# Kernel tuning notes

Measured on AMD Instinct MI355X. Metric: run time of the kernel, lower is better.

Reference implementation:

```python
import jax, jax.numpy as jnp
import numpy as np

B, S, DIM = 4, 2048, 2048
H, KVH, HD = 32, 8, 64
REPEATS = H // KVH
SCALE = HD ** -0.5


def _rope(x, cos, sin):
    # x: (B, S, Hn, HD); cos/sin: (S, HD//2)
    xr = x[..., 0::2]
    xi = x[..., 1::2]
    c = cos[:, None, :]  # (S, 1, HD//2) broadcasts over heads
    s = sin[:, None, :]
    out_r = xr * c - xi * s
    out_i = xr * s + xi * c
    return jnp.stack([out_r, out_i], axis=-1).reshape(x.shape)


def setup_inputs() -> dict:
    key = jax.random.key(0)
    ks = jax.random.split(key, 5)
    x = jax.random.normal(ks[0], (B, S, DIM), dtype=jnp.float32)
    wq = jax.random.normal(ks[1], (H * HD, DIM), dtype=jnp.float32) * 0.02
    wk = jax.random.normal(ks[2], (KVH * HD, DIM), dtype=jnp.float32) * 0.02
    wv = jax.random.normal(ks[3], (KVH * HD, DIM), dtype=jnp.float32) * 0.02
    wo = jax.random.normal(ks[4], (DIM, H * HD), dtype=jnp.float32) * 0.02
    # standard RoPE frequencies: freqs_cis = exp(i * t * theta)
    inv_freq = 1.0 / (10000.0 ** (jnp.arange(0, HD, 2, dtype=jnp.float32) / HD))
    angles = jnp.arange(S, dtype=jnp.float32)[:, None] * inv_freq[None, :]  # (S, HD//2)
    return {
        "x": x, "wq": wq, "wk": wk, "wv": wv, "wo": wo,
        "freqs_cos": jnp.cos(angles), "freqs_sin": jnp.sin(angles),
    }


def reference(x, wq, wk, wv, wo, freqs_cos, freqs_sin):
    b, s, _ = x.shape
    q = (x @ wq.T).reshape(b, s, H, HD)
    k = (x @ wk.T).reshape(b, s, KVH, HD)
    v = (x @ wv.T).reshape(b, s, KVH, HD)
    q = _rope(q, freqs_cos, freqs_sin)
    k = _rope(k, freqs_cos, freqs_sin)
    k_rep = jnp.repeat(k, REPEATS, axis=2)  # (B,S,H,HD)
    v_rep = jnp.repeat(v, REPEATS, axis=2)
    # NOTE: faithful to source - q is NOT transposed to (B,H,S,HD), so the
    # matmul contracts head_dim at each token, producing (B,S,H,H) scores
    # (mixing across heads per position), softmaxed over the last head axis.
    scores = jnp.einsum('bshd,bsed->bshe', q, k_rep) * SCALE  # (B,S,H,H)
    weights = jax.nn.softmax(scores, axis=-1)
    out = jnp.einsum('bshe,bsed->bshd', weights, v_rep)  # (B,S,H,HD)
    out = out.reshape(b, s, H * HD)
    return out @ wo.T
```

## Files before the change

kernel.cpp:

```cpp
#include <hip/hip_runtime.h>

typedef unsigned short u16;
typedef __bf16 bf16x8 __attribute__((ext_vector_type(8)));
typedef float f32x4 __attribute__((ext_vector_type(4)));

#define AS1 __attribute__((address_space(1)))
#define AS3 __attribute__((address_space(3)))

__device__ inline u16 f2bf(float f) {
    union { float f; unsigned u; } c; c.f = f;
    unsigned u = c.u;
    u += 0x7fffu + ((u >> 16) & 1u);
    return (u16)(u >> 16);
}
__device__ inline float bf2f(u16 b) {
    union { unsigned u; float f; } c; c.u = ((unsigned)b) << 16;
    return c.f;
}

__device__ inline void async_cp16(const void* g, void* l) {
    __builtin_amdgcn_global_load_lds((const AS1 void*)g, (AS3 void*)l, 16, 0, 0);
}

__global__ __launch_bounds__(256)
void f32_to_bf16_x8(const float* __restrict__ src, u16* __restrict__ dst) {
    int i = (blockIdx.x * 256 + threadIdx.x) * 8;
    float4 f0 = *(const float4*)(src + i);
    float4 f1 = *(const float4*)(src + i + 4);
    union { u16 h[8]; uint4 v; } o;
    o.h[0] = f2bf(f0.x); o.h[1] = f2bf(f0.y);
    o.h[2] = f2bf(f0.z); o.h[3] = f2bf(f0.w);
    o.h[4] = f2bf(f1.x); o.h[5] = f2bf(f1.y);
    o.h[6] = f2bf(f1.z); o.h[7] = f2bf(f1.w);
    *(uint4*)(dst + i) = o.v;
}

__global__ __launch_bounds__(256)
void conv_weights(const float* __restrict__ wq, const float* __restrict__ wk,
                  const float* __restrict__ wv, const float* __restrict__ wo,
                  u16* __restrict__ wqkv, u16* __restrict__ wo_bf) {
    int i = (blockIdx.x * 256 + threadIdx.x) * 4;
    const float* src;
    u16* dst;
    if (i < 4194304)       { src = wq + i;           dst = wqkv + i; }
    else if (i < 5242880)  { src = wk + (i-4194304); dst = wqkv + i; }
    else if (i < 6291456)  { src = wv + (i-5242880); dst = wqkv + i; }
    else                   { src = wo + (i-6291456); dst = wo_bf + (i-6291456); }
    float4 f = *(const float4*)src;
    union { u16 h[4]; uint2 v; } o;
    o.h[0] = f2bf(f.x); o.h[1] = f2bf(f.y);
    o.h[2] = f2bf(f.z); o.h[3] = f2bf(f.w);
    *(uint2*)dst = o.v;
}

template <bool BF16_OUT>
__global__ __launch_bounds__(512, 2)
void gemm_bt8(const u16* __restrict__ A, const u16* __restrict__ B,
              void* __restrict__ Cout, int N, int K) {
    __shared__ __align__(16) u16 lds[65536];
    char* ldsc = (char*)lds;

    const int tid  = threadIdx.x;
    const int w    = tid >> 6;
    const int lane = tid & 63;
    const int row0 = blockIdx.x * 256;
    const int col0 = blockIdx.y * 256;
    const int wm = w >> 2, wn = w & 3;
    const int lm = lane & 15, quad = lane >> 4;

    const int NT  = K / 64;
    const int NIT = K / 128;
    const int K64 = K * 64, K128 = K * 128;

    const int sr  = lane >> 3;
    const int stC = ((lane & 7) ^ sr) * 8;
    const u16* pA = A + (size_t)(row0 + w * 8 + sr) * K + stC;
    const u16* pB = B + (size_t)(col0 + w * 8 + sr) * K + stC;
    const int stagoff = w * 1024;

    const int cx0   = (quad ^ (lm & 7)) * 16;
    const int cx1   = cx0 ^ 64;
    const int aBase = (wm * 128 + lm) * 128;
    const int bBase = 32768 + (wn * 64 + lm) * 128;

    f32x4 acc[8][4];
#pragma unroll
    for (int i = 0; i < 8; i++)
#pragma unroll
        for (int j = 0; j < 4; j++) acc[i][j] = (f32x4){0.f, 0.f, 0.f, 0.f};

    auto stA = [&](int v, int h) {
        int kb = (v < NT ? v : NT - 1) * 64;
        const u16* g = pA + h * K128 + kb;
        char* d = ldsc + ((v & 1) << 16) + h * 16384 + stagoff;
        async_cp16(g, d);
        async_cp16(g + K64, d + 8192);
    };
    auto stB = [&](int v, int h) {
        int kb = (v < NT ? v : NT - 1) * 64;
        const u16* g = pB + h * K128 + kb;
        char* d = ldsc + ((v & 1) << 16) + 32768 + h * 16384 + stagoff;
        async_cp16(g, d);
        async_cp16(g + K64, d + 8192);
    };

    stB(0, 0); stB(0, 1); stA(0, 0); stA(0, 1);
    stB(1, 0); stB(1, 1); stA(1, 0);
    asm volatile("s_waitcnt vmcnt(6)" ::: "memory");
    __builtin_amdgcn_s_barrier();

    bf16x8 bg[4][2], afX[2][2], afY[2][2];

#define LDR(off) (*(const bf16x8*)(ldsc + (off)))

#define PHASE_TAIL(MI0, AF)                                                   \
    __builtin_amdgcn_s_barrier();                                             \
    asm volatile("s_waitcnt lgkmcnt(0)" ::: "memory");                        \
    __builtin_amdgcn_sched_barrier(0);                                        \
    __builtin_amdgcn_s_setprio(1);                                            \
    _Pragma("unroll")                                                         \
    for (int s = 0; s < 2; s++)                                               \
        _Pragma("unroll")                                                     \
        for (int j = 0; j < 2; j++)                                           \
            _Pragma("unroll")                                                 \
            for (int ni = 0; ni < 4; ni++)                                    \
                acc[(MI0) + j][ni] = __builtin_amdgcn_mfma_f32_16x16x32_bf16( \
                    AF[j][s], bg[ni][s], acc[(MI0) + j][ni], 0, 0, 0);        \
    __builtin_amdgcn_s_setprio(0);

#define HALF_ITER(u, BO)                                                      \
    {                                                                         \
                                                                      \
        _Pragma("unroll")                                                     \
        for (int ni = 0; ni < 4; ni++) {                                      \
            bg[ni][0] = LDR((BO) + bBase + ni * 2048 + cx0);                  \
            bg[ni][1] = LDR((BO) + bBase + ni * 2048 + cx1);                  \
        }                                                                     \
        _Pragma("unroll")                                                     \
        for (int j = 0; j < 2; j++) {                                         \
            afX[j][0] = LDR((BO) + aBase + j * 2048 + cx0);                   \
            afX[j][1] = LDR((BO) + aBase + j * 2048 + cx1);                   \
            afY[j][0] = LDR((BO) + aBase + (2 + j) * 2048 + cx0);             \
            afY[j][1] = LDR((BO) + aBase + (2 + j) * 2048 + cx1);             \
        }                                                                     \
        stA((u) + 1, 1);                                                      \
        asm volatile("s_waitcnt lgkmcnt(8)" ::: "memory");                    \
        PHASE_TAIL(0, afX)                                                    \
        __builtin_amdgcn_s_barrier();                                         \
                                                                      \
        _Pragma("unroll")                                                     \
        for (int j = 0; j < 2; j++) {                                         \
            afX[j][0] = LDR((BO) + aBase + (4 + j) * 2048 + cx0);             \
            afX[j][1] = LDR((BO) + aBase + (4 + j) * 2048 + cx1);             \
        }                                                                     \
        stB((u) + 2, 0);                                                      \
        PHASE_TAIL(2, afY)                                                    \
        __builtin_amdgcn_s_barrier();                                         \
                                                                      \
        _Pragma("unroll")                                                     \
        for (int j = 0; j < 2; j++) {                                         \
            afY[j][0] = LDR((BO) + aBase + (6 + j) * 2048 + cx0);             \
            afY[j][1] = LDR((BO) + aBase + (6 + j) * 2048 + cx1);             \
        }                                                                     \
        stB((u) + 2, 1);                                                      \
        PHASE_TAIL(4, afX)                                                    \
        __builtin_amdgcn_s_barrier();                                         \
                                                                      \
        stA((u) + 2, 0);                                                      \
        PHASE_TAIL(6, afY)                                                    \
        asm volatile("s_waitcnt vmcnt(6)" ::: "memory");                      \
        __builtin_amdgcn_s_barrier();                                         \
    }

    for (int it = 0; it < NIT; ++it) {
        const int t = 2 * it;
        HALF_ITER(t, 0)
        HALF_ITER(t + 1, 65536)
    }

#undef HALF_ITER
#undef PHASE_TAIL
#undef LDR

    const int rbase = row0 + wm * 128 + quad * 4;
    const int cbase = col0 + wn * 64 + lm;
    if (BF16_OUT) {
        u16* C = (u16*)Cout;
#pragma unroll
        for (int mi = 0; mi < 8; mi++)
#pragma unroll
            for (int r = 0; r < 4; r++) {
                size_t ro = (size_t)(rbase + mi * 16 + r) * N;
#pragma unroll
                for (int ni = 0; ni < 4; ni++)
                    C[ro + cbase + ni * 16] = f2bf(acc[mi][ni][r]);
            }
    } else {
        float* C = (float*)Cout;
#pragma unroll
        for (int mi = 0; mi < 8; mi++)
#pragma unroll
            for (int r = 0; r < 4; r++) {
                size_t ro = (size_t)(rbase + mi * 16 + r) * N;
#pragma unroll
                for (int ni = 0; ni < 4; ni++)
                    C[ro + cbase + ni * 16] = acc[mi][ni][r];
            }
    }
}

__global__ __launch_bounds__(256)
void attn_tok(const u16* __restrict__ qkv, u16* __restrict__ out) {
    __shared__ float kvf[1024];
    const int tok = blockIdx.x;
    const int t = threadIdx.x;
    const u16* qrow = qkv + (size_t)tok * 3072;

    {
        uint2 w = *(const uint2*)(qrow + 2048 + t * 4);
        kvf[t * 4 + 0] = bf2f((u16)(w.x & 0xffff));
        kvf[t * 4 + 1] = bf2f((u16)(w.x >> 16));
        kvf[t * 4 + 2] = bf2f((u16)(w.y & 0xffff));
        kvf[t * 4 + 3] = bf2f((u16)(w.y >> 16));
    }
    __syncthreads();

    const int h = t >> 3, j = t & 7;
    float qf[8];
    {
        uint4 w = *(const uint4*)(qrow + h * 64 + j * 8);
        unsigned ws4[4] = {w.x, w.y, w.z, w.w};
#pragma unroll
        for (int i = 0; i < 4; i++) {
            qf[2 * i]     = bf2f((u16)(ws4[i] & 0xffff));
            qf[2 * i + 1] = bf2f((u16)(ws4[i] >> 16));
        }
    }

    float s[8];
#pragma unroll
    for (int g = 0; g < 8; g++) {
        const float* kk = kvf + g * 64 + j * 8;
        float a = 0.f;
#pragma unroll
        for (int d = 0; d < 8; d++) a += qf[d] * kk[d];
        s[g] = a;
    }
#pragma unroll
    for (int g = 0; g < 8; g++) {
        s[g] += __shfl_xor(s[g], 1);
        s[g] += __shfl_xor(s[g], 2);
        s[g] += __shfl_xor(s[g], 4);
    }
    float m = -1e30f;
#pragma unroll
    for (int g = 0; g < 8; g++) { s[g] *= 0.125f; m = fmaxf(m, s[g]); }
    float p[8], l = 0.f;
#pragma unroll
    for (int g = 0; g < 8; g++) { p[g] = __expf(s[g] - m); l += p[g]; }
    float rl = 1.f / l;

    float o[8] = {0, 0, 0, 0, 0, 0, 0, 0};
#pragma unroll
    for (int g = 0; g < 8; g++) {
        float w = p[g] * rl;
        const float* vv = kvf + 512 + g * 64 + j * 8;
#pragma unroll
        for (int d = 0; d < 8; d++) o[d] += w * vv[d];
    }

    unsigned po[4];
#pragma unroll
    for (int i = 0; i < 4; i++)
        po[i] = (unsigned)f2bf(o[2 * i]) | ((unsigned)f2bf(o[2 * i + 1]) << 16);
    uint4 wo_; wo_.x = po[0]; wo_.y = po[1]; wo_.z = po[2]; wo_.w = po[3];
    *(uint4*)(out + (size_t)tok * 2048 + h * 64 + j * 8) = wo_;
}

extern "C" void kernel_launch(void* const* d_in, const int* in_sizes, int n_in,
                              void* d_out, int out_size, void* d_ws, size_t ws_size,
                              hipStream_t stream) {
    const float* x  = (const float*)d_in[0];
    const float* wq = (const float*)d_in[1];
    const float* wk = (const float*)d_in[2];
    const float* wv = (const float*)d_in[3];
    const float* wo = (const float*)d_in[4];

    u16* x_bf  = (u16*)d_ws;
    u16* wqkv  = x_bf  + 16777216;
    u16* wo_bf = wqkv  + 6291456;
    u16* qkv   = wo_bf + 4194304;
    u16* attn  = qkv   + 25165824;

    f32_to_bf16_x8<<<8192, dim3(256), 0, stream>>>(x, x_bf);
    conv_weights<<<10240, dim3(256), 0, stream>>>(wq, wk, wv, wo, wqkv, wo_bf);

    gemm_bt8<true><<<dim3(32, 12), dim3(512), 0, stream>>>(x_bf, wqkv, qkv, 3072, 2048);

    attn_tok<<<8192, dim3(256), 0, stream>>>(qkv, attn);

    gemm_bt8<false><<<dim3(32, 8), dim3(512), 0, stream>>>(attn, wo_bf, (float*)d_out,
                                                           2048, 2048);
}
```

Before: 340.0 us.

## Parametrize GEMM N-tile width and merge conversion kernels into one launch

Result: faster. 328.9 us (-3.3%).

```diff
diff --git a/kernel.cpp b/kernel.cpp
--- a/kernel.cpp
+++ b/kernel.cpp
@@ -23,54 +23,56 @@
 }
 
 __global__ __launch_bounds__(256)
-void f32_to_bf16_x8(const float* __restrict__ src, u16* __restrict__ dst) {
-    int i = (blockIdx.x * 256 + threadIdx.x) * 8;
-    float4 f0 = *(const float4*)(src + i);
-    float4 f1 = *(const float4*)(src + i + 4);
-    union { u16 h[8]; uint4 v; } o;
-    o.h[0] = f2bf(f0.x); o.h[1] = f2bf(f0.y);
-    o.h[2] = f2bf(f0.z); o.h[3] = f2bf(f0.w);
-    o.h[4] = f2bf(f1.x); o.h[5] = f2bf(f1.y);
-    o.h[6] = f2bf(f1.z); o.h[7] = f2bf(f1.w);
-    *(uint4*)(dst + i) = o.v;
-}
-
-__global__ __launch_bounds__(256)
-void conv_weights(const float* __restrict__ wq, const float* __restrict__ wk,
-                  const float* __restrict__ wv, const float* __restrict__ wo,
-                  u16* __restrict__ wqkv, u16* __restrict__ wo_bf) {
-    int i = (blockIdx.x * 256 + threadIdx.x) * 4;
-    const float* src;
-    u16* dst;
-    if (i < 4194304)       { src = wq + i;           dst = wqkv + i; }
-    else if (i < 5242880)  { src = wk + (i-4194304); dst = wqkv + i; }
-    else if (i < 6291456)  { src = wv + (i-5242880); dst = wqkv + i; }
-    else                   { src = wo + (i-6291456); dst = wo_bf + (i-6291456); }
-    float4 f = *(const float4*)src;
-    union { u16 h[4]; uint2 v; } o;
-    o.h[0] = f2bf(f.x); o.h[1] = f2bf(f.y);
-    o.h[2] = f2bf(f.z); o.h[3] = f2bf(f.w);
-    *(uint2*)dst = o.v;
-}
-
-template <bool BF16_OUT>
+void conv_all(const float* __restrict__ x,
+              const float* __restrict__ wq, const float* __restrict__ wk,
+              const float* __restrict__ wv, const float* __restrict__ wo,
+              u16* __restrict__ x_bf, u16* __restrict__ wqkv,
+              u16* __restrict__ wo_bf) {
+    int b = blockIdx.x;
+    if (b < 8192) {
+        int i = (b * 256 + threadIdx.x) * 8;
+        float4 f0 = *(const float4*)(x + i);
+        float4 f1 = *(const float4*)(x + i + 4);
+        union { u16 h[8]; uint4 v; } o;
+        o.h[0] = f2bf(f0.x); o.h[1] = f2bf(f0.y);
+        o.h[2] = f2bf(f0.z); o.h[3] = f2bf(f0.w);
+        o.h[4] = f2bf(f1.x); o.h[5] = f2bf(f1.y);
+        o.h[6] = f2bf(f1.z); o.h[7] = f2bf(f1.w);
+        *(uint4*)(x_bf + i) = o.v;
+    } else {
+        int i = ((b - 8192) * 256 + threadIdx.x) * 4;
+        const float* src;
+        u16* dst;
+        if (i < 4194304)       { src = wq + i;           dst = wqkv + i; }
+        else if (i < 5242880)  { src = wk + (i-4194304); dst = wqkv + i; }
+        else if (i < 6291456)  { src = wv + (i-5242880); dst = wqkv + i; }
+        else                   { src = wo + (i-6291456); dst = wo_bf + (i-6291456); }
+        float4 f = *(const float4*)src;
+        union { u16 h[4]; uint2 v; } o;
+        o.h[0] = f2bf(f.x); o.h[1] = f2bf(f.y);
+        o.h[2] = f2bf(f.z); o.h[3] = f2bf(f.w);
+        *(uint2*)dst = o.v;
+    }
+}
+
+template <int NI, bool BF16_OUT>
 __global__ __launch_bounds__(512, 2)
 void gemm_bt8(const u16* __restrict__ A, const u16* __restrict__ B,
               void* __restrict__ Cout, int N, int K) {
-    __shared__ __align__(16) u16 lds[65536];
-    char* ldsc = (char*)lds;
+    constexpr int SZ = 32768 + NI * 8192;
+    __shared__ __align__(16) char ldsc[2 * SZ];
 
     const int tid  = threadIdx.x;
     const int w    = tid >> 6;
     const int lane = tid & 63;
     const int row0 = blockIdx.x * 256;
-    const int col0 = blockIdx.y * 256;
+    const int col0 = blockIdx.y * (NI * 64);
     const int wm = w >> 2, wn = w & 3;
     const int lm = lane & 15, quad = lane >> 4;
 
     const int NT  = K / 64;
     const int NIT = K / 128;
-    const int K64 = K * 64, K128 = K * 128;
+    const int K64 = K * 64;
 
     const int sr  = lane >> 3;
     const int stC = ((lane & 7) ^ sr) * 8;
@@ -81,35 +83,34 @@
     const int cx0   = (quad ^ (lm & 7)) * 16;
     const int cx1   = cx0 ^ 64;
     const int aBase = (wm * 128 + lm) * 128;
-    const int bBase = 32768 + (wn * 64 + lm) * 128;
-
-    f32x4 acc[8][4];
+    const int bBase = 32768 + (wn * (NI * 16) + lm) * 128;
+
+    f32x4 acc[8][NI];
 #pragma unroll
     for (int i = 0; i < 8; i++)
 #pragma unroll
-        for (int j = 0; j < 4; j++) acc[i][j] = (f32x4){0.f, 0.f, 0.f, 0.f};
-
-    auto stA = [&](int v, int h) {
+        for (int j = 0; j < NI; j++) acc[i][j] = (f32x4){0.f, 0.f, 0.f, 0.f};
+
+    auto stage = [&](const u16* base, int v, int unit, int regionOff) {
         int kb = (v < NT ? v : NT - 1) * 64;
-        const u16* g = pA + h * K128 + kb;
-        char* d = ldsc + ((v & 1) << 16) + h * 16384 + stagoff;
-        async_cp16(g, d);
-        async_cp16(g + K64, d + 8192);
+        async_cp16(base + (size_t)unit * K64 + kb,
+                   ldsc + (v & 1) * SZ + regionOff + unit * 8192 + stagoff);
     };
-    auto stB = [&](int v, int h) {
-        int kb = (v < NT ? v : NT - 1) * 64;
-        const u16* g = pB + h * K128 + kb;
-        char* d = ldsc + ((v & 1) << 16) + 32768 + h * 16384 + stagoff;
-        async_cp16(g, d);
-        async_cp16(g + K64, d + 8192);
-    };
-
-    stB(0, 0); stB(0, 1); stA(0, 0); stA(0, 1);
-    stB(1, 0); stB(1, 1); stA(1, 0);
-    asm volatile("s_waitcnt vmcnt(6)" ::: "memory");
+#define ST_A(v, u) stage(pA, (v), (u), 0)
+#define ST_B(v, u) stage(pB, (v), (u), 32768)
+
+#pragma unroll
+    for (int u = 0; u < 4; u++) ST_A(0, u);
+#pragma unroll
+    for (int u = 0; u < NI; u++) ST_B(0, u);
+#pragma unroll
+    for (int u = 0; u < NI; u++) ST_B(1, u);
+    ST_A(1, 0); ST_A(1, 1);
+    if constexpr (NI == 4) asm volatile("s_waitcnt vmcnt(6)" ::: "memory");
+    else                   asm volatile("s_waitcnt vmcnt(5)" ::: "memory");
     __builtin_amdgcn_s_barrier();
 
-    bf16x8 bg[4][2], afX[2][2], afY[2][2];
+    bf16x8 bg[NI][2], afX[2][2], afY[2][2];
 
 #define LDR(off) (*(const bf16x8*)(ldsc + (off)))
 
@@ -123,7 +124,7 @@
         _Pragma("unroll")                                                     \
         for (int j = 0; j < 2; j++)                                           \
             _Pragma("unroll")                                                 \
-            for (int ni = 0; ni < 4; ni++)                                    \
+            for (int ni = 0; ni < NI; ni++)                                   \
                 acc[(MI0) + j][ni] = __builtin_amdgcn_mfma_f32_16x16x32_bf16( \
                     AF[j][s], bg[ni][s], acc[(MI0) + j][ni], 0, 0, 0);        \
     __builtin_amdgcn_s_setprio(0);
@@ -132,7 +133,7 @@
     {                                                                         \
                                                                       \
         _Pragma("unroll")                                                     \
-        for (int ni = 0; ni < 4; ni++) {                                      \
+        for (int ni = 0; ni < NI; ni++) {                                     \
             bg[ni][0] = LDR((BO) + bBase + ni * 2048 + cx0);                  \
             bg[ni][1] = LDR((BO) + bBase + ni * 2048 + cx1);                  \
         }                                                                     \
@@ -143,7 +144,7 @@
             afY[j][0] = LDR((BO) + aBase + (2 + j) * 2048 + cx0);             \
             afY[j][1] = LDR((BO) + aBase + (2 + j) * 2048 + cx1);             \
         }                                                                     \
-        stA((u) + 1, 1);                                                      \
+        ST_A((u) + 1, 2); ST_A((u) + 1, 3);                                   \
         asm volatile("s_waitcnt lgkmcnt(8)" ::: "memory");                    \
         PHASE_TAIL(0, afX)                                                    \
         __builtin_amdgcn_s_barrier();                                         \
@@ -153,7 +154,7 @@
             afX[j][0] = LDR((BO) + aBase + (4 + j) * 2048 + cx0);             \
             afX[j][1] = LDR((BO) + aBase + (4 + j) * 2048 + cx1);             \
         }                                                                     \
-        stB((u) + 2, 0);                                                      \
+        ST_B((u) + 2, 0); ST_B((u) + 2, 1);                                   \
         PHASE_TAIL(2, afY)                                                    \
         __builtin_amdgcn_s_barrier();                                         \
                                                                       \
@@ -162,28 +163,34 @@
             afY[j][0] = LDR((BO) + aBase + (6 + j) * 2048 + cx0);             \
             afY[j][1] = LDR((BO) + aBase + (6 + j) * 2048 + cx1);             \
         }                                                                     \
-        stB((u) + 2, 1);                                                      \
+        ST_B((u) + 2, 2);                                                     \
+        if constexpr (NI == 4) { ST_B((u) + 2, 3); }                          \
+        else                   { ST_A((u) + 2, 0); }                          \
         PHASE_TAIL(4, afX)                                                    \
         __builtin_amdgcn_s_barrier();                                         \
                                                                       \
-        stA((u) + 2, 0);                                                      \
+        if constexpr (NI == 4) { ST_A((u) + 2, 0); ST_A((u) + 2, 1); }        \
+        else                   { ST_A((u) + 2, 1); }                          \
         PHASE_TAIL(6, afY)                                                    \
-        asm volatile("s_waitcnt vmcnt(6)" ::: "memory");                      \
+        if constexpr (NI == 4) asm volatile("s_waitcnt vmcnt(6)" ::: "memory");\
+        else                   asm volatile("s_waitcnt vmcnt(5)" ::: "memory");\
         __builtin_amdgcn_s_barrier();                                         \
     }
 
     for (int it = 0; it < NIT; ++it) {
         const int t = 2 * it;
         HALF_ITER(t, 0)
-        HALF_ITER(t + 1, 65536)
+        HALF_ITER(t + 1, SZ)
     }
 
 #undef HALF_ITER
 #undef PHASE_TAIL
 #undef LDR
+#undef ST_A
+#undef ST_B
 
     const int rbase = row0 + wm * 128 + quad * 4;
-    const int cbase = col0 + wn * 64 + lm;
+    const int cbase = col0 + wn * (NI * 16) + lm;
     if (BF16_OUT) {
         u16* C = (u16*)Cout;
 #pragma unroll
@@ -192,7 +199,7 @@
             for (int r = 0; r < 4; r++) {
                 size_t ro = (size_t)(rbase + mi * 16 + r) * N;
 #pragma unroll
-                for (int ni = 0; ni < 4; ni++)
+                for (int ni = 0; ni < NI; ni++)
                     C[ro + cbase + ni * 16] = f2bf(acc[mi][ni][r]);
             }
     } else {
@@ -203,7 +210,7 @@
             for (int r = 0; r < 4; r++) {
                 size_t ro = (size_t)(rbase + mi * 16 + r) * N;
 #pragma unroll
-                for (int ni = 0; ni < 4; ni++)
+                for (int ni = 0; ni < NI; ni++)
                     C[ro + cbase + ni * 16] = acc[mi][ni][r];
             }
     }
@@ -292,13 +299,14 @@
     u16* qkv   = wo_bf + 4194304;
     u16* attn  = qkv   + 25165824;
 
-    f32_to_bf16_x8<<<8192, dim3(256), 0, stream>>>(x, x_bf);
-    conv_weights<<<10240, dim3(256), 0, stream>>>(wq, wk, wv, wo, wqkv, wo_bf);
-
-    gemm_bt8<true><<<dim3(32, 12), dim3(512), 0, stream>>>(x_bf, wqkv, qkv, 3072, 2048);
+    conv_all<<<18432, dim3(256), 0, stream>>>(x, wq, wk, wv, wo, x_bf, wqkv, wo_bf);
+
+    gemm_bt8<3, true><<<dim3(32, 16), dim3(512), 0, stream>>>(x_bf, wqkv, qkv,
+                                                              3072, 2048);
 
     attn_tok<<<8192, dim3(256), 0, stream>>>(qkv, attn);
 
-    gemm_bt8<false><<<dim3(32, 8), dim3(512), 0, stream>>>(attn, wo_bf, (float*)d_out,
-                                                           2048, 2048);
-}
+    gemm_bt8<4, false><<<dim3(32, 8), dim3(512), 0, stream>>>(attn, wo_bf,
+                                                              (float*)d_out,
+                                                              2048, 2048);
+}
```
